# Kernel tuning notes

Measured on AMD Instinct MI355X. Metric: run time of the kernel, lower is better.

## Reference

```python
import jax, jax.numpy as jnp
import numpy as np

H_IMG, W_IMG = 64, 64          # token grid (n = H*W = 4096)
D_MODEL = 512
N_HEADS = 8
D1 = 1024                      # expand_ratio * d_model, multiple of n_heads
HEAD_DIM = D1 // N_HEADS       # 128
RANK = 32
NK = 16                        # inducing points for SKI interpolation


def interp_weights(n, nk):
    # inverse-time warp: position i -> 1/(i+1) in (0,1], linearly interpolated
    # onto nk uniform inducing points in [0,1] (2 nonzeros per row).
    pos = 1.0 / (jnp.arange(n, dtype=jnp.float32) + 1.0)
    t = pos * (nk - 1)
    idx = jnp.clip(jnp.floor(t).astype(jnp.int32), 0, nk - 2)
    frac = t - idx.astype(jnp.float32)
    r = jnp.arange(n)
    Wm = jnp.zeros((n, nk), jnp.float32)
    Wm = Wm.at[r, idx].set(1.0 - frac).at[r, idx + 1].set(frac)
    return Wm  # (n, nk)


def apply_toep(v, U, V):
    # v: (b, m, n, h, d); low-rank SKI Toeplitz mixing along axis n.
    # T ~= (Wm @ U) (Wm @ V)^T per head  -> O(n*r*d) instead of O(n^2*d).
    n = v.shape[2]
    nk = U.shape[1]
    Wm = interp_weights(n, nk)                      # (n, nk)
    A = jnp.einsum('nk,hkr->hnr', Wm, U)            # (h, n, r)
    B = jnp.einsum('nk,hkr->hnr', Wm, V)            # (h, n, r)
    tmp = jnp.einsum('hnr,bmnhd->bmhrd', B, v)      # contract over n
    return jnp.einsum('hnr,bmhrd->bmnhd', A, tmp)


def setup_inputs() -> dict:
    key = jax.random.key(0)
    ks = jax.random.split(key, 12)
    s = 0.02
    x = jax.random.normal(ks[0], (16, H_IMG * W_IMG, D_MODEL), jnp.float32)
    Wu = s * jax.random.normal(ks[1], (D1, D_MODEL), jnp.float32)
    bu = s * jax.random.normal(ks[2], (D1,), jnp.float32)
    Wv = s * jax.random.normal(ks[3], (D1, D_MODEL), jnp.float32)
    bv = s * jax.random.normal(ks[4], (D1,), jnp.float32)
    Wo = s * jax.random.normal(ks[5], (D_MODEL, D1), jnp.float32)
    bo = s * jax.random.normal(ks[6], (D_MODEL,), jnp.float32)
    U1 = s * jax.random.normal(ks[7], (N_HEADS, NK, RANK), jnp.float32)
    V1 = s * jax.random.normal(ks[8], (N_HEADS, NK, RANK), jnp.float32)
    U2 = s * jax.random.normal(ks[9], (N_HEADS, NK, RANK), jnp.float32)
    V2 = s * jax.random.normal(ks[10], (N_HEADS, NK, RANK), jnp.float32)
    return {'x': x, 'Wu': Wu, 'bu': bu, 'Wv': Wv, 'bv': bv, 'Wo': Wo,
            'bo': bo, 'U1': U1, 'V1': V1, 'U2': U2, 'V2': V2}


def reference(x, Wu, bu, Wv, bv, Wo, bo, U1, V1, U2, V2):
    b, n, _ = x.shape
    H = int(np.sqrt(n)); W = n // H
    u = jax.nn.silu(x @ Wu.T + bu)                  # (b, n, d1)
    v = jax.nn.silu(x @ Wv.T + bv)                  # (b, n, d1)
    v4 = v.reshape(b, H, W, N_HEADS, HEAD_DIM)      # (b, H, W, h, d)

    # o1: toep1 along W, then toep2 along H
    t = apply_toep(v4, U1, V1)                      # mix along W
    t = t.transpose(0, 2, 1, 3, 4)                  # (b, W, H, h, d)
    t = apply_toep(t, U2, V2)                       # mix along H
    o1 = t.transpose(0, 2, 1, 3, 4)

    # o2: toep2 along H, then toep1 along W
    s_ = v4.transpose(0, 2, 1, 3, 4)                # (b, W, H, h, d)
    s_ = apply_toep(s_, U2, V2)                     # mix along H
    s_ = s_.transpose(0, 2, 1, 3, 4)                # (b, H, W, h, d)
    o2 = apply_toep(s_, U1, V1)                     # mix along W

    out = (o1 + o2).reshape(b, n, D1)
    out = u * out                                   # gated token mixing
    return out @ Wo.T + bo                          # (b, n, d_model)
```

## Files before the change

kernel.cpp:

```cpp
#include <hip/hip_runtime.h>
#include <hip/hip_bf16.h>

typedef unsigned short u16;
typedef unsigned int   u32;
typedef float  f32x4  __attribute__((ext_vector_type(4)));
typedef __bf16 bf16x8 __attribute__((ext_vector_type(8)));
typedef u16    u16x8  __attribute__((ext_vector_type(8)));
typedef u16    u16x4  __attribute__((ext_vector_type(4)));

__device__ __forceinline__ u16 f2bf(float f) {
  u32 x = __builtin_bit_cast(u32, f);
  x += 0x7fffu + ((x >> 16) & 1u);
  return (u16)(x >> 16);
}
__device__ __forceinline__ float bf2f(u16 u) {
  return __builtin_bit_cast(float, (u32)u << 16);
}
__device__ __forceinline__ void gload_lds16(const u16* g, u16* l) {
  __builtin_amdgcn_global_load_lds(
      (const __attribute__((address_space(1))) void*)g,
      (__attribute__((address_space(3))) void*)l, 16, 0, 0);
}

__global__ void k_conv_x(const float* __restrict__ x, u16* __restrict__ xb) {
  int g = blockIdx.x * 256 + threadIdx.x;
  const float4* src = (const float4*)(x + (size_t)g * 8);
  float4 f0 = src[0], f1 = src[1];
  u16x8 o;
  o[0]=f2bf(f0.x); o[1]=f2bf(f0.y); o[2]=f2bf(f0.z); o[3]=f2bf(f0.w);
  o[4]=f2bf(f1.x); o[5]=f2bf(f1.y); o[6]=f2bf(f1.z); o[7]=f2bf(f1.w);
  *(u16x8*)(xb + (size_t)g * 8) = o;
}

__global__ void k_conv_w(const float* __restrict__ Wu, const float* __restrict__ Wv,
                         const float* __restrict__ Wo, const float* __restrict__ bu,
                         const float* __restrict__ bv, u16* __restrict__ wuvb,
                         u16* __restrict__ wob, float* __restrict__ biasuv) {
  int g = blockIdx.x * 256 + threadIdx.x;
  int e = g * 4;
  const float* src; u16* dst;
  if (e < 524288)        { src = Wu + e;             dst = wuvb + e; }
  else if (e < 1048576)  { src = Wv + (e - 524288);  dst = wuvb + e; }
  else                   { src = Wo + (e - 1048576); dst = wob + (e - 1048576); }
  float4 f = *(const float4*)src;
  u16x4 o; o[0]=f2bf(f.x); o[1]=f2bf(f.y); o[2]=f2bf(f.z); o[3]=f2bf(f.w);
  *(u16x4*)dst = o;
  if (g < 2048) biasuv[g] = (g < 1024) ? bu[g] : bv[g - 1024];
}

__global__ void k_toep(const float* __restrict__ U1, const float* __restrict__ V1,
                       const float* __restrict__ U2, const float* __restrict__ V2,
                       u16* __restrict__ T1b, u16* __restrict__ T2b) {
  __shared__ float Us[512], Vs[512];
  int bid = blockIdx.x, t = threadIdx.x;
  int which = bid >> 6, rest = bid & 63, h = rest >> 3, seg = rest & 7;
  const float* U = which ? U2 : U1;
  const float* V = which ? V2 : V1;
  u16* T = which ? T2b : T1b;
  float scale = which ? 2.0f : 1.0f;
  for (int i = t; i < 512; i += 256) { Us[i] = U[h*512 + i]; Vs[i] = V[h*512 + i]; }
  __syncthreads();
  for (int q = 0; q < 2; ++q) {
    int e = seg * 512 + q * 256 + t;
    int i = e >> 6, j = e & 63;
    float pi = 1.0f / (float)(i + 1); float tvi = pi * 15.0f;
    int ii = min((int)floorf(tvi), 14); float fi = tvi - (float)ii;
    float pj = 1.0f / (float)(j + 1); float tvj = pj * 15.0f;
    int jj = min((int)floorf(tvj), 14); float fj = tvj - (float)jj;
    float s = 0.0f;
    #pragma unroll
    for (int r = 0; r < 32; ++r) {
      float a = (1.0f - fi) * Us[ii*32 + r] + fi * Us[(ii+1)*32 + r];
      float b = (1.0f - fj) * Vs[jj*32 + r] + fj * Vs[(jj+1)*32 + r];
      s += a * b;
    }
    T[h*4096 + i*64 + j] = f2bf(s * scale);
  }
}

template<int EPI, int K, int LGNBN, int LDC>
__global__ __launch_bounds__(256, 3) void k_gemm128(
    const u16* __restrict__ A, const u16* __restrict__ B,
    const float* __restrict__ bias, void* __restrict__ C) {
  __shared__ alignas(16) u16 As[128 * 64];
  __shared__ alignas(16) u16 Bs[128 * 64];
  const int t = threadIdx.x, l = t & 63, w = t >> 6;
  const int wm = (w >> 1) << 6, wn = (w & 1) << 6;
  const int nwg = gridDim.x;
  const int lb = (blockIdx.x & 7) * (nwg >> 3) + (blockIdx.x >> 3);
  const int bn = lb & ((1 << LGNBN) - 1), bm = lb >> LGNBN;
  const u16* Ab = A + (size_t)bm * 128 * K;
  const u16* Bb = B + (size_t)bn * 128 * K;

  f32x4 acc[4][4];
  #pragma unroll
  for (int i = 0; i < 4; ++i)
    #pragma unroll
    for (int j = 0; j < 4; ++j) acc[i][j] = (f32x4){0.f, 0.f, 0.f, 0.f};

  for (int kt = 0; kt < K; kt += 64) {
    #pragma unroll
    for (int q = 0; q < 4; ++q) {
      int idx = q * 256 + t;
      int rr = idx >> 3, s8 = idx & 7;
      int col = (s8 ^ (rr & 7)) << 3;
      gload_lds16(Ab + (size_t)rr * K + kt + col, &As[idx * 8]);
    }
    #pragma unroll
    for (int q = 0; q < 4; ++q) {
      int idx = q * 256 + t;
      int rr = idx >> 3, s8 = idx & 7;
      int col = (s8 ^ (rr & 7)) << 3;
      gload_lds16(Bb + (size_t)rr * K + kt + col, &Bs[idx * 8]);
    }
    asm volatile("s_waitcnt vmcnt(0)");
    __syncthreads();
    #pragma unroll
    for (int ks = 0; ks < 2; ++ks) {
      bf16x8 af[4], bfr[4];
      int q8 = ks * 4 + (l >> 4);
      #pragma unroll
      for (int mf = 0; mf < 4; ++mf) {
        int R = wm + mf * 16 + (l & 15);
        af[mf] = *(const bf16x8*)&As[R * 64 + ((q8 ^ (R & 7)) << 3)];
      }
      #pragma unroll
      for (int nf = 0; nf < 4; ++nf) {
        int R = wn + nf * 16 + (l & 15);
        bfr[nf] = *(const bf16x8*)&Bs[R * 64 + ((q8 ^ (R & 7)) << 3)];
      }
      #pragma unroll
      for (int mf = 0; mf < 4; ++mf)
        #pragma unroll
        for (int nf = 0; nf < 4; ++nf)
          acc[mf][nf] = __builtin_amdgcn_mfma_f32_16x16x32_bf16(
              af[mf], bfr[nf], acc[mf][nf], 0, 0, 0);
    }
    __syncthreads();
  }

  #pragma unroll
  for (int mf = 0; mf < 4; ++mf) {
    int gm0 = bm * 128 + wm + mf * 16 + (l >> 4) * 4;
    #pragma unroll
    for (int nf = 0; nf < 4; ++nf) {
      int gn = bn * 128 + wn + nf * 16 + (l & 15);
      float bi = bias[gn];
      #pragma unroll
      for (int r = 0; r < 4; ++r) {
        float z = acc[mf][nf][r] + bi;
        size_t off = (size_t)(gm0 + r) * LDC + gn;
        if (EPI == 0) {
          z = z / (1.0f + __expf(-z));
          ((u16*)C)[off] = f2bf(z);
        } else {
          ((float*)C)[off] = z;
        }
      }
    }
  }
}

template<int PASS>
__global__ __launch_bounds__(256) void k_mix(const u16* __restrict__ uv,
                                             u16* __restrict__ y,
                                             const u16* __restrict__ Tmat) {
  __shared__ alignas(16) u16 Ts[64 * 72];
  __shared__ alignas(16) u32 VT[128 * 36];
  int bid = blockIdx.x, t = threadIdx.x;
  int h = bid & 7, outer = (bid >> 3) & 63, b = bid >> 9;
  int l = t & 63, w = t >> 6;

  {
    const u16* Tg = Tmat + h * 4096;
    int rr = t >> 2, cc = (t & 3) * 16;
    const uint4* src = (const uint4*)(Tg + rr * 64 + cc);
    uint4 v0 = src[0], v1 = src[1];
    *(uint4*)&Ts[rr * 72 + cc] = v0;
    *(uint4*)&Ts[rr * 72 + cc + 8] = v1;
  }

  size_t inbase; size_t instride;
  if (PASS == 0) { inbase = ((size_t)(b*64 + outer) * 64) * 2048 + 1024 + h*128; instride = 2048; }
  else           { inbase = ((size_t)b * 4096 + outer) * 1024 + h*128;            instride = 65536; }
  const u16* inp = (PASS == 0) ? uv : (const u16*)y;

  #pragma unroll
  for (int a2 = 0; a2 < 2; ++a2) {
    int jp = (t >> 4) + a2 * 16;
    int dc = t & 15;
    const u16* r0 = inp + inbase + (size_t)(2*jp) * instride + dc * 8;
    const u16* r1 = r0 + instride;
    uint4 av = *(const uint4*)r0;
    uint4 bv = *(const uint4*)r1;
    u32 a4[4] = {av.x, av.y, av.z, av.w};
    u32 b4[4] = {bv.x, bv.y, bv.z, bv.w};
    #pragma unroll
    for (int ww = 0; ww < 4; ++ww) {
      u32 lo = (a4[ww] & 0xffffu) | (b4[ww] << 16);
      u32 hi = (a4[ww] >> 16) | (b4[ww] & 0xffff0000u);
      int d0 = dc * 8 + 2 * ww, d1 = d0 + 1;
      VT[d0 * 36 + (jp ^ ((((u32)d0 >> 3) & 7) << 2))] = lo;
      VT[d1 * 36 + (jp ^ ((((u32)d1 >> 3) & 7) << 2))] = hi;
    }
  }
  __syncthreads();

  f32x4 acc[8];
  #pragma unroll
  for (int nf = 0; nf < 8; ++nf) acc[nf] = (f32x4){0.f, 0.f, 0.f, 0.f};
  #pragma unroll
  for (int ks = 0; ks < 2; ++ks) {
    bf16x8 af = *(const bf16x8*)&Ts[(w*16 + (l & 15)) * 72 + ks*32 + (l >> 4)*8];
    #pragma unroll
    for (int nf = 0; nf < 8; ++nf) {
      int d  = nf * 16 + (l & 15);
      int kd = ks * 16 + (l >> 4) * 4;
      u32 dw = (u32)d * 36 + ((u32)kd ^ ((((u32)d >> 3) & 7) << 2));
      bf16x8 bfv = *(const bf16x8*)&VT[dw];
      acc[nf] = __builtin_amdgcn_mfma_f32_16x16x32_bf16(af, bfv, acc[nf], 0, 0, 0);
    }
  }

  size_t obase, ostride, ubase = 0;
  if (PASS == 0) { obase = ((size_t)(b*64 + outer) * 64) * 1024 + h*128; ostride = 1024; }
  else {
    obase = ((size_t)b * 4096 + outer) * 1024 + h*128; ostride = 65536;
    ubase = ((size_t)b * 4096 + outer) * 2048 + h*128;
  }
  #pragma unroll
  for (int nf = 0; nf < 8; ++nf) {
    int d = nf * 16 + (l & 15);
    #pragma unroll
    for (int r = 0; r < 4; ++r) {
      int m = w * 16 + (l >> 4) * 4 + r;
      float val = acc[nf][r];
      if (PASS == 1) val *= bf2f(uv[ubase + (size_t)m * 131072 + d]);
      y[obase + (size_t)m * ostride + d] = f2bf(val);
    }
  }
}

extern "C" void kernel_launch(void* const* d_in, const int* in_sizes, int n_in,
                              void* d_out, int out_size, void* d_ws, size_t ws_size,
                              hipStream_t stream) {
  const float* x  = (const float*)d_in[0];
  const float* Wu = (const float*)d_in[1];
  const float* bu = (const float*)d_in[2];
  const float* Wv = (const float*)d_in[3];
  const float* bv = (const float*)d_in[4];
  const float* Wo = (const float*)d_in[5];
  const float* bo = (const float*)d_in[6];
  const float* U1 = (const float*)d_in[7];
  const float* V1 = (const float*)d_in[8];
  const float* U2 = (const float*)d_in[9];
  const float* V2 = (const float*)d_in[10];
  float* out = (float*)d_out;

  char* p = (char*)d_ws;
  u16*  xb     = (u16*)(p + 0);
  u16*  wuvb   = (u16*)(p + 67108864);
  u16*  wob    = (u16*)(p + 69206016);
  u16*  T1b    = (u16*)(p + 70254592);
  u16*  T2b    = (u16*)(p + 70320128);
  float* biasuv= (float*)(p + 70385664);
  u16*  uv     = (u16*)(p + 70393856);
  u16*  y      = (u16*)(p + 338829312);
  if (ws_size < 473047040ULL) return;

  k_conv_x<<<16384, 256, 0, stream>>>(x, xb);
  k_conv_w<<<1536, 256, 0, stream>>>(Wu, Wv, Wo, bu, bv, wuvb, wob, biasuv);
  k_toep<<<128, 256, 0, stream>>>(U1, V1, U2, V2, T1b, T2b);
  k_gemm128<0, 512, 4, 2048><<<8192, 256, 0, stream>>>(xb, wuvb, biasuv, (void*)uv);
  k_mix<0><<<8192, 256, 0, stream>>>(uv, y, T1b);
  k_mix<1><<<8192, 256, 0, stream>>>(uv, y, T2b);
  k_gemm128<1, 1024, 2, 512><<<2048, 256, 0, stream>>>(y, wob, bo, (void*)out);
}
```

Before: 527.7 us.

## Double-buffer GEMM LDS tiles with K=32 stages and async prefetch

Splits the GEMM K loop into 32-wide tiles held in two LDS buffers. The load for tile+2 is issued while the current tile is computed, using partial vmcnt waits so global-to-LDS copies overlap the MFMA work. The swizzle is adapted to 32-column rows and the launch-bounds occupancy hint is raised from 3 to 5. It adds more barriers per unit of K and halves the MFMA work per barrier. The waitcnt accounting and buffer reuse ordering carry correctness risk.

```diff
diff --git a/kernel.cpp b/kernel.cpp
--- a/kernel.cpp
+++ b/kernel.cpp
@@ -79,11 +79,12 @@
 }
 
 template<int EPI, int K, int LGNBN, int LDC>
-__global__ __launch_bounds__(256, 3) void k_gemm128(
+__global__ __launch_bounds__(256, 5) void k_gemm128(
     const u16* __restrict__ A, const u16* __restrict__ B,
     const float* __restrict__ bias, void* __restrict__ C) {
-  __shared__ alignas(16) u16 As[128 * 64];
-  __shared__ alignas(16) u16 Bs[128 * 64];
+  constexpr int NT = K >> 5;
+  __shared__ alignas(16) u16 As[2][4096];
+  __shared__ alignas(16) u16 Bs[2][4096];
   const int t = threadIdx.x, l = t & 63, w = t >> 6;
   const int wm = (w >> 1) << 6, wn = (w & 1) << 6;
   const int nwg = gridDim.x;
@@ -98,46 +99,57 @@
     #pragma unroll
     for (int j = 0; j < 4; ++j) acc[i][j] = (f32x4){0.f, 0.f, 0.f, 0.f};
 
-  for (int kt = 0; kt < K; kt += 64) {
-    #pragma unroll
-    for (int q = 0; q < 4; ++q) {
-      int idx = q * 256 + t;
-      int rr = idx >> 3, s8 = idx & 7;
-      int col = (s8 ^ (rr & 7)) << 3;
-      gload_lds16(Ab + (size_t)rr * K + kt + col, &As[idx * 8]);
-    }
-    #pragma unroll
-    for (int q = 0; q < 4; ++q) {
-      int idx = q * 256 + t;
-      int rr = idx >> 3, s8 = idx & 7;
-      int col = (s8 ^ (rr & 7)) << 3;
-      gload_lds16(Bb + (size_t)rr * K + kt + col, &Bs[idx * 8]);
-    }
-    asm volatile("s_waitcnt vmcnt(0)");
-    __syncthreads();
-    #pragma unroll
-    for (int ks = 0; ks < 2; ++ks) {
-      bf16x8 af[4], bfr[4];
-      int q8 = ks * 4 + (l >> 4);
+#define STAGE(T) do {                                                        \
+    int _t = (T);                                                            \
+    size_t _kt = (size_t)_t << 5;                                            \
+    u16* _dA = &As[_t & 1][0];                                               \
+    u16* _dB = &Bs[_t & 1][0];                                               \
+    _Pragma("unroll")                                                        \
+    for (int _j = 0; _j < 2; ++_j) {                                         \
+      int _idx = _j * 256 + t;                                               \
+      int _rr = _idx >> 2, _s = _idx & 3;                                    \
+      int _col = (_s ^ ((_rr >> 2) & 3)) << 3;                               \
+      gload_lds16(Ab + (size_t)_rr * K + _kt + _col, _dA + _idx * 8);        \
+      gload_lds16(Bb + (size_t)_rr * K + _kt + _col, _dB + _idx * 8);        \
+    }                                                                        \
+  } while (0)
+
+  STAGE(0); STAGE(1);
+  asm volatile("s_waitcnt vmcnt(4)");
+  __builtin_amdgcn_s_barrier();
+
+  for (int tile = 0; tile < NT; ++tile) {
+    const u16* Asb = &As[tile & 1][0];
+    const u16* Bsb = &Bs[tile & 1][0];
+    const int ksl = l >> 4;
+    bf16x8 af[4], bfr[4];
+    #pragma unroll
+    for (int mf = 0; mf < 4; ++mf) {
+      int R = wm + mf * 16 + (l & 15);
+      af[mf] = *(const bf16x8*)&Asb[R * 32 + ((ksl ^ ((R >> 2) & 3)) << 3)];
+    }
+    #pragma unroll
+    for (int nf = 0; nf < 4; ++nf) {
+      int R = wn + nf * 16 + (l & 15);
+      bfr[nf] = *(const bf16x8*)&Bsb[R * 32 + ((ksl ^ ((R >> 2) & 3)) << 3)];
+    }
+    #pragma unroll
+    for (int mf = 0; mf < 4; ++mf)
       #pragma unroll
-      for (int mf = 0; mf < 4; ++mf) {
-        int R = wm + mf * 16 + (l & 15);
-        af[mf] = *(const bf16x8*)&As[R * 64 + ((q8 ^ (R & 7)) << 3)];
-      }
-      #pragma unroll
-      for (int nf = 0; nf < 4; ++nf) {
-        int R = wn + nf * 16 + (l & 15);
-        bfr[nf] = *(const bf16x8*)&Bs[R * 64 + ((q8 ^ (R & 7)) << 3)];
-      }
-      #pragma unroll
-      for (int mf = 0; mf < 4; ++mf)
-        #pragma unroll
-        for (int nf = 0; nf < 4; ++nf)
-          acc[mf][nf] = __builtin_amdgcn_mfma_f32_16x16x32_bf16(
-              af[mf], bfr[nf], acc[mf][nf], 0, 0, 0);
-    }
-    __syncthreads();
-  }
+      for (int nf = 0; nf < 4; ++nf)
+        acc[mf][nf] = __builtin_amdgcn_mfma_f32_16x16x32_bf16(
+            af[mf], bfr[nf], acc[mf][nf], 0, 0, 0);
+    __builtin_amdgcn_s_barrier();
+    if (tile + 2 < NT) {
+      STAGE(tile + 2);
+      asm volatile("s_waitcnt vmcnt(4)");
+      __builtin_amdgcn_s_barrier();
+    } else if (tile + 1 < NT) {
+      asm volatile("s_waitcnt vmcnt(0)");
+      __builtin_amdgcn_s_barrier();
+    }
+  }
+#undef STAGE
 
   #pragma unroll
   for (int mf = 0; mf < 4; ++mf) {
```

Measured after the change: 812.4 us. +53.9%, slower.
